# Performance work log

Hardware: AMD Instinct MI355X
Metric: run time of the kernel (lower is better)

## Reference

```python
import jax, jax.numpy as jnp
import numpy as np

NUM_EMBEDDINGS = 16384
EMBEDDING_DIM = 256
B, C, H, W = 8, 256, 32, 32


def _l2_normalize(x, axis=-1, eps=1e-12):
    # matches torch.nn.functional.normalize(p=2): x / max(||x||, eps)
    n = jnp.sqrt(jnp.sum(x * x, axis=axis, keepdims=True))
    return x / jnp.maximum(n, eps)


def setup_inputs() -> dict:
    key = jax.random.key(0)
    k1, k2 = jax.random.split(key)
    z = jax.random.normal(k1, (B, C, H, W), dtype=jnp.float32)
    embedding_weight = jax.random.normal(k2, (NUM_EMBEDDINGS, EMBEDDING_DIM), dtype=jnp.float32)
    return {"z": z, "embedding_weight": embedding_weight}


def reference(z, embedding_weight):
    batch_size, channels, height, width = z.shape
    # [B,C,H,W] -> [B,H,W,C] -> [N, D]
    z_flat = jnp.transpose(z, (0, 2, 3, 1)).reshape(-1, EMBEDDING_DIM)
    z_flat = _l2_normalize(z_flat)                 # l2_norm=True
    emb = _l2_normalize(embedding_weight)
    # squared distances: ||z||^2 + ||e||^2 - 2 z e^T  -> [N, K]
    d = (jnp.sum(z_flat * z_flat, axis=1, keepdims=True)
         + jnp.sum(emb * emb, axis=1)
         - 2.0 * jnp.matmul(z_flat, emb.T))
    indices = jnp.argmin(d, axis=1)                # [N]
    z_q = emb[indices].reshape(batch_size, height, width, EMBEDDING_DIM)
    z_q = jnp.transpose(z_q, (0, 3, 1, 2))         # [B,C,H,W]
    indices = indices.reshape(batch_size, height, width)
    return z_q, indices
```

## Files before the change

kernel.cpp:

```cpp
#include <hip/hip_runtime.h>

#define NUM_E   16384
#define DIM     256
#define NROWS   8192
#define HW      1024
#define BM      128
#define BN      256
#define NCB     (NUM_E / BN)
#define GATE    2.5e-3f
#define TAUC    2.5e-3f
#define EHID    2.5e-3
#define MAXC    16

typedef __bf16 bf16x8 __attribute__((ext_vector_type(8)));
typedef float  f32x16 __attribute__((ext_vector_type(16)));

__device__ __forceinline__ unsigned short f2bf(float x) {
    unsigned u = __float_as_uint(x);
    unsigned r = (u + 0x7fffu + ((u >> 16) & 1u)) >> 16;
    return (unsigned short)r;
}
__device__ __forceinline__ int imax(int a, int b) { return a > b ? a : b; }
__device__ __forceinline__ int imin(int a, int b) { return a < b ? a : b; }
__device__ __forceinline__ bf16x8 ld16(const unsigned short* p) {
    return *(const bf16x8*)p;
}
__device__ __forceinline__ size_t faddr(int row, int kk) {
    return ((size_t)((row >> 5) * 16 + (kk >> 4))) * 512
         + ((row & 31) + ((kk >> 3) & 1) * 32) * 8 + (kk & 7);
}

__global__ void k_pre(const float* __restrict__ z, const float* __restrict__ emb,
                      float* __restrict__ zpart, float* __restrict__ inv_e,
                      double* __restrict__ se2, unsigned short* __restrict__ Eh,
                      int* __restrict__ cnt, int* __restrict__ cnt2) {
    int bid = blockIdx.x;
    if (bid < NUM_E / 4) {
        if (bid == 0 && threadIdx.x == 0) { *cnt = 0; *cnt2 = 0; }
        int wv = threadIdx.x >> 6, lane = threadIdx.x & 63;
        int k = bid * 4 + wv;
        float4 v = *(const float4*)(emb + (size_t)k * DIM + lane * 4);
        double sq = (double)v.x*v.x + (double)v.y*v.y + (double)v.z*v.z + (double)v.w*v.w;
        for (int off = 32; off > 0; off >>= 1) sq += __shfl_down(sq, off);
        double tot = fmax(__shfl(sq, 0), 1e-24);
        if (lane == 0) { se2[k] = tot; inv_e[k] = 1.0f / fmaxf((float)sqrt(tot), 1e-12f); }
        float s = 1.0f / fmaxf((float)sqrt(tot), 1e-12f);
        ushort4 h;
        h.x = f2bf(v.x * s); h.y = f2bf(v.y * s); h.z = f2bf(v.z * s); h.w = f2bf(v.w * s);
        *(ushort4*)(Eh + faddr(k, lane * 4)) = h;
    } else {
        int ib = bid - NUM_E / 4;
        int n = (ib & 31) * 256 + threadIdx.x;
        int cb = ib >> 5;
        int b = n >> 10, hw = n & 1023;
        const float* p = z + (size_t)(b * DIM + cb * 16) * HW + hw;
        float s = 0.f;
        #pragma unroll
        for (int c = 0; c < 16; c++) { float v = p[c * HW]; s += v * v; }
        zpart[cb * NROWS + n] = s;
    }
}

__global__ void k_prep_z(const float* __restrict__ z, const float* __restrict__ zpart,
                         unsigned short* __restrict__ Zh) {
    __shared__ float T[64 * 68];
    __shared__ __align__(16) float Tinv[64];
    int t = threadIdx.x;
    int n0 = blockIdx.x * 64, c0 = blockIdx.y * 64;
    int b = n0 >> 10, hw0 = n0 & 1023;
    if (t < 64) {
        float s = 0.f;
        #pragma unroll
        for (int cb = 0; cb < 16; cb++) s += zpart[cb * NROWS + n0 + t];
        Tinv[t] = 1.0f / fmaxf(sqrtf(s), 1e-12f);
    }
    __syncthreads();
    #pragma unroll
    for (int i = 0; i < 4; i++) {
        int f = t + 256 * i;
        int cc = f >> 4, n4 = (f & 15) * 4;
        float4 v  = *(const float4*)(z + (size_t)(b * DIM + c0 + cc) * HW + hw0 + n4);
        float4 iv = *(const float4*)&Tinv[n4];
        v.x *= iv.x; v.y *= iv.y; v.z *= iv.z; v.w *= iv.w;
        *(float4*)&T[cc * 68 + n4] = v;
    }
    __syncthreads();
    #pragma unroll
    for (int i = 0; i < 4; i++) {
        int f = t + 256 * i;
        int nn = f >> 4, c4 = (f & 15) * 4;
        ushort4 h;
        h.x = f2bf(T[(c4+0)*68 + nn]);
        h.y = f2bf(T[(c4+1)*68 + nn]);
        h.z = f2bf(T[(c4+2)*68 + nn]);
        h.w = f2bf(T[(c4+3)*68 + nn]);
        *(ushort4*)(Zh + faddr(n0 + nn, c0 + c4)) = h;
    }
}

__launch_bounds__(256, 2)
__global__ void k_score(const unsigned short* __restrict__ Zh,
                        const unsigned short* __restrict__ Eh, int2* __restrict__ part) {
    __shared__ __align__(16) int kv[8448];
    const int t = threadIdx.x, l = t & 63, w = t >> 6;
    const int wm = w >> 1, wn = w & 1;
    int bid = blockIdx.x;
    int rr2 = (bid & 7) * 512 + (bid >> 3);
    int st = rr2 >> 6, wi = rr2 & 63;
    const int m0 = ((st >> 3) * 8 + (wi >> 3)) * BM;
    const int nb = ((st & 7) * 8 + (wi & 7)) * BN;
    const int l31 = l & 31, lh = l >> 5;

    const unsigned short* pa0 = Zh + ((size_t)((m0 >> 5) + wm * 2 + 0) * 16) * 512 + l * 8;
    const unsigned short* pa1 = Zh + ((size_t)((m0 >> 5) + wm * 2 + 1) * 16) * 512 + l * 8;
    const unsigned short* pb0 = Eh + ((size_t)((nb >> 5) + wn * 4 + 0) * 16) * 512 + l * 8;
    const unsigned short* pb1 = Eh + ((size_t)((nb >> 5) + wn * 4 + 1) * 16) * 512 + l * 8;
    const unsigned short* pb2 = Eh + ((size_t)((nb >> 5) + wn * 4 + 2) * 16) * 512 + l * 8;
    const unsigned short* pb3 = Eh + ((size_t)((nb >> 5) + wn * 4 + 3) * 16) * 512 + l * 8;

    f32x16 acc[2][4];
    #pragma unroll
    for (int i = 0; i < 2; i++)
        #pragma unroll
        for (int j = 0; j < 4; j++) acc[i][j] = (f32x16)2.0f;

    bf16x8 fr[3][6];
#define LDS3(s, OFF) \
    fr[s][0] = ld16(pa0 + (OFF)); fr[s][1] = ld16(pa1 + (OFF)); \
    fr[s][2] = ld16(pb0 + (OFF)); fr[s][3] = ld16(pb1 + (OFF)); \
    fr[s][4] = ld16(pb2 + (OFF)); fr[s][5] = ld16(pb3 + (OFF));

    LDS3(0, 0); LDS3(1, 512);
    #pragma unroll
    for (int ks = 0; ks < 16; ks++) {
        const int s = ks % 3;
        if (ks + 2 < 16) { const int s2 = (ks + 2) % 3; LDS3(s2, (ks + 2) * 512); }
        __builtin_amdgcn_s_setprio(1);
        #pragma unroll
        for (int i = 0; i < 2; i++)
            #pragma unroll
            for (int j = 0; j < 4; j++)
                acc[i][j] = __builtin_amdgcn_mfma_f32_32x32x16_bf16(fr[s][i], fr[s][2 + j], acc[i][j], 0, 0, 0);
        __builtin_amdgcn_s_setprio(0);
    }
#undef LDS3

    const int colbase = wn * 128 + l31;
    int KA1 = 0, KA2 = 0, KB1 = 0, KB2 = 0;
    const int rl = t >> 2, q = t & 3;
    #pragma unroll
    for (int i = 0; i < 2; i++) {
        #pragma unroll
        for (int reg = 0; reg < 16; reg++) {
            int k0 = (__float_as_int(acc[i][0][reg]) & 0xFFFFFF00) | colbase;
            int k1 = (__float_as_int(acc[i][1][reg]) & 0xFFFFFF00) | (colbase + 32);
            int k2 = (__float_as_int(acc[i][2][reg]) & 0xFFFFFF00) | (colbase + 64);
            int k3 = (__float_as_int(acc[i][3][reg]) & 0xFFFFFF00) | (colbase + 96);
            int a = imax(k0, k1), b = imin(k0, k1);
            int c = imax(k2, k3), d = imin(k2, k3);
            int K1 = imax(a, c);
            int K2 = imax(imin(a, c), imax(b, d));
            int rr = wm * 32 + (reg & 3) + 8 * (reg >> 2) + 4 * lh;
            int slot = wn * 32 + l31;
            *(int2*)&kv[(rr * 66 + slot) * 2] = make_int2(K1, K2);
        }
        __syncthreads();
        int S1 = 0, S2 = 0;
        const int2* pr = (const int2*)&kv[(rl * 66 + q * 16) * 2];
        #pragma unroll
        for (int u = 0; u < 16; u++) {
            int2 e = pr[u];
            S2 = imax(imax(S2, e.y), imin(S1, e.x));
            S1 = imax(S1, e.x);
        }
        __syncthreads();
        #pragma unroll
        for (int d2 = 1; d2 <= 2; d2 <<= 1) {
            int o1 = __shfl_down(S1, d2), o2 = __shfl_down(S2, d2);
            S2 = imax(imax(S2, o2), imin(S1, o1));
            S1 = imax(S1, o1);
        }
        if (i == 0) { KA1 = S1; KA2 = S2; } else { KB1 = S1; KB2 = S2; }
    }
    if ((t & 3) == 0) {
        int rowA = (rl >> 5) * 64 + (rl & 31);
        int rowB = rowA + 32;
        int seg = nb / BN;
        part[(size_t)seg * NROWS + m0 + rowA] = make_int2(KA1, KA2);
        part[(size_t)seg * NROWS + m0 + rowB] = make_int2(KB1, KB2);
    }
}

__global__ void k_final(const int2* __restrict__ part, int* __restrict__ idx_ws,
                        float* __restrict__ out_idx, int* __restrict__ flags,
                        int* __restrict__ cnt, int* __restrict__ cand,
                        int* __restrict__ ccnt, float* __restrict__ v2q) {
    __shared__ int rK1[8][33], rK2[8][33], rS[8][33];
    __shared__ int bK1[32], bK2[32];
    __shared__ int lcc[32];
    __shared__ int lcand[32][MAXC];
    __shared__ int sv2[8][33];
    const int nl = threadIdx.x & 31, sc = threadIdx.x >> 5;
    const int n = blockIdx.x * 32 + nl;
    if (threadIdx.x < 32) lcc[threadIdx.x] = 0;
    int K1 = 0, K2 = 0, S1 = 0;
    for (int s = sc * 8; s < sc * 8 + 8; s++) {
        int2 e = part[(size_t)s * NROWS + n];
        S1 = (e.x > K1) ? s : S1;
        int nK2 = imax(imin(K1, e.x), imax(K2, e.y));
        K1 = imax(K1, e.x);
        K2 = nK2;
    }
    rK1[sc][nl] = K1; rK2[sc][nl] = K2; rS[sc][nl] = S1;
    __syncthreads();
    if (threadIdx.x < 32) {
        int W1 = 0, W2 = 0, WS = 0;
        #pragma unroll
        for (int s2 = 0; s2 < 8; s2++) {
            int e1 = rK1[s2][threadIdx.x], e2 = rK2[s2][threadIdx.x];
            WS = (e1 > W1) ? rS[s2][threadIdx.x] : WS;
            int nW2 = imax(imin(W1, e1), imax(W2, e2));
            W1 = imax(W1, e1);
            W2 = nW2;
        }
        int nn = blockIdx.x * 32 + threadIdx.x;
        int J1 = WS * BN + (W1 & 0xFF);
        idx_ws[nn] = J1;
        out_idx[nn] = (float)J1;
        bK1[threadIdx.x] = W1;
        bK2[threadIdx.x] = W2;
    }
    __syncthreads();
    int kthr = __float_as_int(__int_as_float(bK1[nl] & 0xFFFFFF00) - TAUC);
    int lv2 = 0;
    for (int s = sc * 8; s < sc * 8 + 8; s++) {
        int2 e = part[(size_t)s * NROWS + n];
        if (e.x >= kthr) {
            int pos = atomicAdd(&lcc[nl], 2);
            if (pos < MAXC)     lcand[nl][pos]     = s * BN + (e.x & 0xFF);
            if (pos + 1 < MAXC) lcand[nl][pos + 1] = s * BN + (e.y & 0xFF);
            lv2 = imax(lv2, e.y);
        }
    }
    sv2[sc][nl] = lv2;
    __syncthreads();
    if (threadIdx.x < 32) {
        int nn = blockIdx.x * 32 + threadIdx.x;
        float v1 = __int_as_float(bK1[threadIdx.x] & 0xFFFFFF00) - 2.0f;
        float v2 = __int_as_float(bK2[threadIdx.x] & 0xFFFFFF00) - 2.0f;
        if (v1 - v2 < GATE) {
            int m = 0;
            #pragma unroll
            for (int s2 = 0; s2 < 8; s2++) m = imax(m, sv2[s2][threadIdx.x]);
            int p = atomicAdd(cnt, 1);
            flags[p] = nn;
            ccnt[nn] = lcc[threadIdx.x];
            v2q[nn] = __int_as_float(m & 0xFFFFFF00) - 2.0f;
            #pragma unroll
            for (int j = 0; j < MAXC; j++) cand[nn * MAXC + j] = lcand[threadIdx.x][j];
        }
    }
}

__launch_bounds__(256)
__global__ void k_rescan_cand(const int* __restrict__ flags, const int* __restrict__ cnt,
                              const int* __restrict__ cand, const int* __restrict__ ccnt,
                              const float* __restrict__ v2q,
                              const float* __restrict__ z, const float* __restrict__ emb,
                              const double* __restrict__ se2,
                              int* __restrict__ idx_ws, float* __restrict__ out_idx,
                              int* __restrict__ flags2, int* __restrict__ cnt2) {
    __shared__ double zs[DIM];
    __shared__ double wv[4];
    __shared__ int    wi[4];
    const int t = threadIdx.x, l = t & 63, w = t >> 6;
    const int F = *cnt;
    for (int f = blockIdx.x; f < F; f += gridDim.x) {
        int n = flags[f];
        int C = ccnt[n];
        int b = n >> 10, hw = n & 1023;
        __syncthreads();
        zs[t] = (double)z[(size_t)(b * DIM + t) * HW + hw];
        __syncthreads();
        double best = -2e18; int bi = 0x7fffffff;
        if (C <= MAXC) {
            double z0 = zs[l*4], z1 = zs[l*4+1], z2 = zs[l*4+2], z3 = zs[l*4+3];
            for (int cix = w; cix < C; cix += 4) {
                int k = cand[n * MAXC + cix];
                float4 ev = *(const float4*)(emb + (size_t)k * DIM + l * 4);
                double d = z0 * (double)ev.x + z1 * (double)ev.y
                         + z2 * (double)ev.z + z3 * (double)ev.w;
                #pragma unroll
                for (int o = 32; o > 0; o >>= 1) d += __shfl_down(d, o);
                if (l == 0) {
                    double qv = d / sqrt(se2[k]);
                    if (qv > best || (qv == best && k < bi)) { best = qv; bi = k; }
                }
            }
        }
        if (l == 0) { wv[w] = best; wi[w] = bi; }
        __syncthreads();
        if (t == 0) {
            if (C > MAXC) {
                int p = atomicAdd(cnt2, 1); flags2[p] = n;
            } else {
                double B = wv[0]; int BI = wi[0];
                #pragma unroll
                for (int x = 1; x < 4; x++)
                    if (wv[x] > B || (wv[x] == B && wi[x] < BI)) { B = wv[x]; BI = wi[x]; }
                if ((double)v2q[n] >= B - EHID) {
                    int p = atomicAdd(cnt2, 1); flags2[p] = n;
                } else {
                    idx_ws[n] = BI; out_idx[n] = (float)BI;
                }
            }
        }
    }
}

__launch_bounds__(256)
__global__ void k_fullscan_part(const int* __restrict__ flags2, const int* __restrict__ cnt2,
                                const float* __restrict__ z, const float* __restrict__ emb,
                                const double* __restrict__ se2, double2* __restrict__ partial) {
    __shared__ double zs[DIM];
    __shared__ double wv[4];
    __shared__ int    wi[4];
    const int t = threadIdx.x, l = t & 63, w = t >> 6;
    const int W = (*cnt2) * 64;
    for (int item = blockIdx.x; item < W; item += gridDim.x) {
        int f = item >> 6, split = item & 63;
        int n = flags2[f];
        int b = n >> 10, hw = n & 1023;
        __syncthreads();
        zs[t] = (double)z[(size_t)(b * DIM + t) * HW + hw];
        __syncthreads();
        double z0 = zs[l*4], z1 = zs[l*4+1], z2 = zs[l*4+2], z3 = zs[l*4+3];
        double best = -2e18; int bi = 0;
        int kbase = split * 256 + w * 64;
        for (int p = 0; p < 64; p++) {
            int k = kbase + p;
            float4 ev = *(const float4*)(emb + (size_t)k * DIM + l * 4);
            double d = z0 * (double)ev.x + z1 * (double)ev.y
                     + z2 * (double)ev.z + z3 * (double)ev.w;
            #pragma unroll
            for (int o = 32; o > 0; o >>= 1) d += __shfl_down(d, o);
            if (l == 0) {
                double qv = d / sqrt(se2[k]);
                if (qv > best) { best = qv; bi = k; }
            }
        }
        if (l == 0) { wv[w] = best; wi[w] = bi; }
        __syncthreads();
        if (t == 0) {
            double B = wv[0]; int BI = wi[0];
            #pragma unroll
            for (int x = 1; x < 4; x++)
                if (wv[x] > B || (wv[x] == B && wi[x] < BI)) { B = wv[x]; BI = wi[x]; }
            partial[item] = make_double2(B, (double)BI);
        }
        __syncthreads();
    }
}

__global__ void k_fullscan_merge(const int* __restrict__ flags2, const int* __restrict__ cnt2,
                                 const double2* __restrict__ partial,
                                 int* __restrict__ idx_ws, float* __restrict__ out_idx) {
    const int F = *cnt2;
    const int l = threadIdx.x & 63, w = threadIdx.x >> 6;
    for (int f = blockIdx.x * 4 + w; f < F; f += gridDim.x * 4) {
        double2 e = partial[(size_t)f * 64 + l];
        double v = e.x; int i = (int)e.y;
        #pragma unroll
        for (int o = 32; o > 0; o >>= 1) {
            double ov = __shfl_down(v, o);
            int    oi = __shfl_down(i, o);
            if (ov > v || (ov == v && oi < i)) { v = ov; i = oi; }
        }
        if (l == 0) { int n = flags2[f]; idx_ws[n] = i; out_idx[n] = (float)i; }
    }
}

__global__ void k_zq(const int* __restrict__ idx_ws, const float* __restrict__ emb,
                     const float* __restrict__ inv_e, float* __restrict__ zq) {
    int t = threadIdx.x;
    int n = blockIdx.x * 256 + t;
    int b = n >> 10, hw = n & 1023;
    int c0 = blockIdx.y * 32;
    int id = idx_ws[n];
    float s = inv_e[id];
    const float* er = emb + (size_t)id * DIM;
    #pragma unroll
    for (int cc = 0; cc < 32; cc += 4) {
        float4 a = *(const float4*)(er + c0 + cc);
        zq[(size_t)(b * DIM + c0 + cc + 0) * HW + hw] = a.x * s;
        zq[(size_t)(b * DIM + c0 + cc + 1) * HW + hw] = a.y * s;
        zq[(size_t)(b * DIM + c0 + cc + 2) * HW + hw] = a.z * s;
        zq[(size_t)(b * DIM + c0 + cc + 3) * HW + hw] = a.w * s;
    }
}

extern "C" void kernel_launch(void* const* d_in, const int* in_sizes, int n_in,
                              void* d_out, int out_size, void* d_ws, size_t ws_size,
                              hipStream_t stream) {
    const float* z   = (const float*)d_in[0];
    const float* emb = (const float*)d_in[1];

    unsigned short* Zh = (unsigned short*)d_ws;
    unsigned short* Eh = Zh + (size_t)NROWS * DIM;
    float*  inv_e = (float*)(Eh + (size_t)NUM_E * DIM);
    float*  zpart = inv_e + NUM_E;
    int*    idx_ws = (int*)(zpart + 16 * NROWS);
    double* se2   = (double*)(idx_ws + NROWS);
    int*    flags = (int*)(se2 + NUM_E);
    int*    flags2 = flags + NROWS;
    int*    cand  = flags2 + NROWS;
    int*    ccnt  = cand + NROWS * MAXC;
    float*  v2q   = (float*)(ccnt + NROWS);
    int*    cnt   = (int*)(v2q + NROWS);
    int*    cnt2  = cnt + 1;

    float* zq      = (float*)d_out;
    float* out_idx = zq + (size_t)NROWS * DIM;
    int2*    part    = (int2*)zq;
    double2* partial = (double2*)zq;

    k_pre    <<<NUM_E / 4 + 512, 256, 0, stream>>>(z, emb, zpart, inv_e, se2, Eh, cnt, cnt2);
    k_prep_z <<<dim3(NROWS / 64, DIM / 64), 256, 0, stream>>>(z, zpart, Zh);
    k_score  <<<(NROWS / BM) * NCB, 256, 0, stream>>>(Zh, Eh, part);
    k_final  <<<NROWS / 32, 256, 0, stream>>>(part, idx_ws, out_idx, flags, cnt,
                                              cand, ccnt, v2q);
    k_rescan_cand  <<<1024, 256, 0, stream>>>(flags, cnt, cand, ccnt, v2q, z, emb,
                                              se2, idx_ws, out_idx, flags2, cnt2);
    k_fullscan_part<<<2048, 256, 0, stream>>>(flags2, cnt2, z, emb, se2, partial);
    k_fullscan_merge<<<64, 256, 0, stream>>>(flags2, cnt2, partial, idx_ws, out_idx);
    k_zq     <<<dim3(NROWS / 256, 8), 256, 0, stream>>>(idx_ws, emb, inv_e, zq);
}
```

Measured before the change: 170.1 us.

## Fuse candidate rescan into final reduction and merge full-scan via atomicMax

Folds the candidate rescan into the per-row final reduction kernel, so candidate lists stay in shared memory instead of making a global round trip. Replaces the full-scan partial buffer and its separate merge kernel with a packed 64-bit atomicMax per row, which k_zq decodes. This removes two kernel launches and the intermediate global traffic. In exchange, the rescan work becomes serialized within each 32-row block, and the packed key truncates the low mantissa bits of the score.

```diff
diff --git a/kernel.cpp b/kernel.cpp
--- a/kernel.cpp
+++ b/kernel.cpp
@@ -29,14 +29,18 @@
     return ((size_t)((row >> 5) * 16 + (kk >> 4))) * 512
          + ((row & 31) + ((kk >> 3) & 1) * 32) * 8 + (kk & 7);
 }
+__device__ __forceinline__ unsigned long long packqv(double qv, int k) {
+    return (((unsigned long long)__double_as_longlong(qv + 2.0)) & ~0x3FFFull)
+         | (unsigned long long)(0x3FFF - k);
+}
 
 __global__ void k_pre(const float* __restrict__ z, const float* __restrict__ emb,
                       float* __restrict__ zpart, float* __restrict__ inv_e,
                       double* __restrict__ se2, unsigned short* __restrict__ Eh,
-                      int* __restrict__ cnt, int* __restrict__ cnt2) {
+                      int* __restrict__ cnt2) {
     int bid = blockIdx.x;
     if (bid < NUM_E / 4) {
-        if (bid == 0 && threadIdx.x == 0) { *cnt = 0; *cnt2 = 0; }
+        if (bid == 0 && threadIdx.x == 0) { *cnt2 = 0; }
         int wv = threadIdx.x >> 6, lane = threadIdx.x & 63;
         int k = bid * 4 + wv;
         float4 v = *(const float4*)(emb + (size_t)k * DIM + lane * 4);
@@ -191,18 +195,28 @@
     }
 }
 
-__global__ void k_final(const int2* __restrict__ part, int* __restrict__ idx_ws,
-                        float* __restrict__ out_idx, int* __restrict__ flags,
-                        int* __restrict__ cnt, int* __restrict__ cand,
-                        int* __restrict__ ccnt, float* __restrict__ v2q) {
+__global__ void k_resolve(const int2* __restrict__ part, int* __restrict__ idx_ws,
+                          float* __restrict__ out_idx,
+                          const float* __restrict__ z, const float* __restrict__ emb,
+                          const double* __restrict__ se2,
+                          int* __restrict__ flags2, int* __restrict__ cnt2,
+                          unsigned long long* __restrict__ slot, int* __restrict__ bm) {
     __shared__ int rK1[8][33], rK2[8][33], rS[8][33];
     __shared__ int bK1[32], bK2[32];
     __shared__ int lcc[32];
     __shared__ int lcand[32][MAXC];
     __shared__ int sv2[8][33];
-    const int nl = threadIdx.x & 31, sc = threadIdx.x >> 5;
+    __shared__ int rescueList[32];
+    __shared__ float v2s[32];
+    __shared__ int nRescue;
+    __shared__ double zs[DIM];
+    __shared__ double wv[4];
+    __shared__ int    wi[4];
+    const int t = threadIdx.x, l = t & 63, w = t >> 6;
+    const int nl = t & 31, sc = t >> 5;
     const int n = blockIdx.x * 32 + nl;
-    if (threadIdx.x < 32) lcc[threadIdx.x] = 0;
+    if (t < 32) lcc[t] = 0;
+    if (t == 0) nRescue = 0;
     int K1 = 0, K2 = 0, S1 = 0;
     for (int s = sc * 8; s < sc * 8 + 8; s++) {
         int2 e = part[(size_t)s * NROWS + n];
@@ -213,22 +227,23 @@
     }
     rK1[sc][nl] = K1; rK2[sc][nl] = K2; rS[sc][nl] = S1;
     __syncthreads();
-    if (threadIdx.x < 32) {
+    if (t < 32) {
         int W1 = 0, W2 = 0, WS = 0;
         #pragma unroll
         for (int s2 = 0; s2 < 8; s2++) {
-            int e1 = rK1[s2][threadIdx.x], e2 = rK2[s2][threadIdx.x];
-            WS = (e1 > W1) ? rS[s2][threadIdx.x] : WS;
+            int e1 = rK1[s2][t], e2 = rK2[s2][t];
+            WS = (e1 > W1) ? rS[s2][t] : WS;
             int nW2 = imax(imin(W1, e1), imax(W2, e2));
             W1 = imax(W1, e1);
             W2 = nW2;
         }
-        int nn = blockIdx.x * 32 + threadIdx.x;
+        int nn = blockIdx.x * 32 + t;
         int J1 = WS * BN + (W1 & 0xFF);
         idx_ws[nn] = J1;
         out_idx[nn] = (float)J1;
-        bK1[threadIdx.x] = W1;
-        bK2[threadIdx.x] = W2;
+        bK1[t] = W1;
+        bK2[t] = W2;
+        bm[nn] = 0;
     }
     __syncthreads();
     int kthr = __float_as_int(__int_as_float(bK1[nl] & 0xFFFFFF00) - TAUC);
@@ -244,41 +259,25 @@
     }
     sv2[sc][nl] = lv2;
     __syncthreads();
-    if (threadIdx.x < 32) {
-        int nn = blockIdx.x * 32 + threadIdx.x;
-        float v1 = __int_as_float(bK1[threadIdx.x] & 0xFFFFFF00) - 2.0f;
-        float v2 = __int_as_float(bK2[threadIdx.x] & 0xFFFFFF00) - 2.0f;
+    if (t < 32) {
+        float v1 = __int_as_float(bK1[t] & 0xFFFFFF00) - 2.0f;
+        float v2 = __int_as_float(bK2[t] & 0xFFFFFF00) - 2.0f;
         if (v1 - v2 < GATE) {
             int m = 0;
             #pragma unroll
-            for (int s2 = 0; s2 < 8; s2++) m = imax(m, sv2[s2][threadIdx.x]);
-            int p = atomicAdd(cnt, 1);
-            flags[p] = nn;
-            ccnt[nn] = lcc[threadIdx.x];
-            v2q[nn] = __int_as_float(m & 0xFFFFFF00) - 2.0f;
-            #pragma unroll
-            for (int j = 0; j < MAXC; j++) cand[nn * MAXC + j] = lcand[threadIdx.x][j];
-        }
-    }
-}
-
-__launch_bounds__(256)
-__global__ void k_rescan_cand(const int* __restrict__ flags, const int* __restrict__ cnt,
-                              const int* __restrict__ cand, const int* __restrict__ ccnt,
-                              const float* __restrict__ v2q,
-                              const float* __restrict__ z, const float* __restrict__ emb,
-                              const double* __restrict__ se2,
-                              int* __restrict__ idx_ws, float* __restrict__ out_idx,
-                              int* __restrict__ flags2, int* __restrict__ cnt2) {
-    __shared__ double zs[DIM];
-    __shared__ double wv[4];
-    __shared__ int    wi[4];
-    const int t = threadIdx.x, l = t & 63, w = t >> 6;
-    const int F = *cnt;
-    for (int f = blockIdx.x; f < F; f += gridDim.x) {
-        int n = flags[f];
-        int C = ccnt[n];
-        int b = n >> 10, hw = n & 1023;
+            for (int s2 = 0; s2 < 8; s2++) m = imax(m, sv2[s2][t]);
+            int r = atomicAdd(&nRescue, 1);
+            rescueList[r] = t;
+            v2s[t] = __int_as_float(m & 0xFFFFFF00) - 2.0f;
+        }
+    }
+    __syncthreads();
+    const int NR = nRescue;
+    for (int ri = 0; ri < NR; ri++) {
+        int lr = rescueList[ri];
+        int nn = blockIdx.x * 32 + lr;
+        int C = lcc[lr];
+        int b = nn >> 10, hw = nn & 1023;
         __syncthreads();
         zs[t] = (double)z[(size_t)(b * DIM + t) * HW + hw];
         __syncthreads();
@@ -286,7 +285,7 @@
         if (C <= MAXC) {
             double z0 = zs[l*4], z1 = zs[l*4+1], z2 = zs[l*4+2], z3 = zs[l*4+3];
             for (int cix = w; cix < C; cix += 4) {
-                int k = cand[n * MAXC + cix];
+                int k = lcand[lr][cix];
                 float4 ev = *(const float4*)(emb + (size_t)k * DIM + l * 4);
                 double d = z0 * (double)ev.x + z1 * (double)ev.y
                          + z2 * (double)ev.z + z3 * (double)ev.w;
@@ -301,27 +300,33 @@
         if (l == 0) { wv[w] = best; wi[w] = bi; }
         __syncthreads();
         if (t == 0) {
-            if (C > MAXC) {
-                int p = atomicAdd(cnt2, 1); flags2[p] = n;
-            } else {
+            bool esc = (C > MAXC);
+            if (!esc) {
                 double B = wv[0]; int BI = wi[0];
                 #pragma unroll
                 for (int x = 1; x < 4; x++)
                     if (wv[x] > B || (wv[x] == B && wi[x] < BI)) { B = wv[x]; BI = wi[x]; }
-                if ((double)v2q[n] >= B - EHID) {
-                    int p = atomicAdd(cnt2, 1); flags2[p] = n;
+                if ((double)v2s[lr] >= B - EHID) {
+                    esc = true;
                 } else {
-                    idx_ws[n] = BI; out_idx[n] = (float)BI;
+                    idx_ws[nn] = BI; out_idx[nn] = (float)BI;
                 }
             }
+            if (esc) {
+                slot[nn] = 0ull;
+                bm[nn] = 1;
+                int p = atomicAdd(cnt2, 1);
+                flags2[p] = nn;
+            }
         }
     }
 }
 
 __launch_bounds__(256)
-__global__ void k_fullscan_part(const int* __restrict__ flags2, const int* __restrict__ cnt2,
-                                const float* __restrict__ z, const float* __restrict__ emb,
-                                const double* __restrict__ se2, double2* __restrict__ partial) {
+__global__ void k_fullscan(const int* __restrict__ flags2, const int* __restrict__ cnt2,
+                           const float* __restrict__ z, const float* __restrict__ emb,
+                           const double* __restrict__ se2,
+                           unsigned long long* __restrict__ slot) {
     __shared__ double zs[DIM];
     __shared__ double wv[4];
     __shared__ int    wi[4];
@@ -346,7 +351,7 @@
             for (int o = 32; o > 0; o >>= 1) d += __shfl_down(d, o);
             if (l == 0) {
                 double qv = d / sqrt(se2[k]);
-                if (qv > best) { best = qv; bi = k; }
+                if (qv > best || (qv == best && k < bi)) { best = qv; bi = k; }
             }
         }
         if (l == 0) { wv[w] = best; wi[w] = bi; }
@@ -356,37 +361,25 @@
             #pragma unroll
             for (int x = 1; x < 4; x++)
                 if (wv[x] > B || (wv[x] == B && wi[x] < BI)) { B = wv[x]; BI = wi[x]; }
-            partial[item] = make_double2(B, (double)BI);
-        }
-        __syncthreads();
-    }
-}
-
-__global__ void k_fullscan_merge(const int* __restrict__ flags2, const int* __restrict__ cnt2,
-                                 const double2* __restrict__ partial,
-                                 int* __restrict__ idx_ws, float* __restrict__ out_idx) {
-    const int F = *cnt2;
-    const int l = threadIdx.x & 63, w = threadIdx.x >> 6;
-    for (int f = blockIdx.x * 4 + w; f < F; f += gridDim.x * 4) {
-        double2 e = partial[(size_t)f * 64 + l];
-        double v = e.x; int i = (int)e.y;
-        #pragma unroll
-        for (int o = 32; o > 0; o >>= 1) {
-            double ov = __shfl_down(v, o);
-            int    oi = __shfl_down(i, o);
-            if (ov > v || (ov == v && oi < i)) { v = ov; i = oi; }
-        }
-        if (l == 0) { int n = flags2[f]; idx_ws[n] = i; out_idx[n] = (float)i; }
+            atomicMax(&slot[n], packqv(B, BI));
+        }
+        __syncthreads();
     }
 }
 
 __global__ void k_zq(const int* __restrict__ idx_ws, const float* __restrict__ emb,
-                     const float* __restrict__ inv_e, float* __restrict__ zq) {
+                     const float* __restrict__ inv_e, float* __restrict__ zq,
+                     const int* __restrict__ bm, const unsigned long long* __restrict__ slot,
+                     float* __restrict__ out_idx) {
     int t = threadIdx.x;
     int n = blockIdx.x * 256 + t;
     int b = n >> 10, hw = n & 1023;
     int c0 = blockIdx.y * 32;
     int id = idx_ws[n];
+    if (bm[n]) {
+        id = 0x3FFF - (int)(slot[n] & 0x3FFFull);
+        if (blockIdx.y == 0) out_idx[n] = (float)id;
+    }
     float s = inv_e[id];
     const float* er = emb + (size_t)id * DIM;
     #pragma unroll
@@ -411,27 +404,21 @@
     float*  zpart = inv_e + NUM_E;
     int*    idx_ws = (int*)(zpart + 16 * NROWS);
     double* se2   = (double*)(idx_ws + NROWS);
-    int*    flags = (int*)(se2 + NUM_E);
-    int*    flags2 = flags + NROWS;
-    int*    cand  = flags2 + NROWS;
-    int*    ccnt  = cand + NROWS * MAXC;
-    float*  v2q   = (float*)(ccnt + NROWS);
-    int*    cnt   = (int*)(v2q + NROWS);
-    int*    cnt2  = cnt + 1;
+    int*    bm    = (int*)(se2 + NUM_E);
+    int*    flags2 = bm + NROWS;
+    int*    cnt2  = flags2 + NROWS;
+    unsigned long long* slot = (unsigned long long*)zpart;
 
     float* zq      = (float*)d_out;
     float* out_idx = zq + (size_t)NROWS * DIM;
-    int2*    part    = (int2*)zq;
-    double2* partial = (double2*)zq;
-
-    k_pre    <<<NUM_E / 4 + 512, 256, 0, stream>>>(z, emb, zpart, inv_e, se2, Eh, cnt, cnt2);
-    k_prep_z <<<dim3(NROWS / 64, DIM / 64), 256, 0, stream>>>(z, zpart, Zh);
-    k_score  <<<(NROWS / BM) * NCB, 256, 0, stream>>>(Zh, Eh, part);
-    k_final  <<<NROWS / 32, 256, 0, stream>>>(part, idx_ws, out_idx, flags, cnt,
-                                              cand, ccnt, v2q);
-    k_rescan_cand  <<<1024, 256, 0, stream>>>(flags, cnt, cand, ccnt, v2q, z, emb,
-                                              se2, idx_ws, out_idx, flags2, cnt2);
-    k_fullscan_part<<<2048, 256, 0, stream>>>(flags2, cnt2, z, emb, se2, partial);
-    k_fullscan_merge<<<64, 256, 0, stream>>>(flags2, cnt2, partial, idx_ws, out_idx);
-    k_zq     <<<dim3(NROWS / 256, 8), 256, 0, stream>>>(idx_ws, emb, inv_e, zq);
-}
+    int2* part = (int2*)zq;
+
+    k_pre     <<<NUM_E / 4 + 512, 256, 0, stream>>>(z, emb, zpart, inv_e, se2, Eh, cnt2);
+    k_prep_z  <<<dim3(NROWS / 64, DIM / 64), 256, 0, stream>>>(z, zpart, Zh);
+    k_score   <<<(NROWS / BM) * NCB, 256, 0, stream>>>(Zh, Eh, part);
+    k_resolve <<<NROWS / 32, 256, 0, stream>>>(part, idx_ws, out_idx, z, emb, se2,
+                                               flags2, cnt2, slot, bm);
+    k_fullscan<<<2048, 256, 0, stream>>>(flags2, cnt2, z, emb, se2, slot);
+    k_zq      <<<dim3(NROWS / 256, 8), 256, 0, stream>>>(idx_ws, emb, inv_e, zq,
+                                                         bm, slot, out_idx);
+}
```

Measured after the change: 179.9 us. 5.8% more time.
